# Optimization experiments

Hardware: AMD Instinct MI355X
Metric: run time of the kernel (lower is better)

## Reference

```python
import jax, jax.numpy as jnp
import numpy as np

B, N, D, H = 4, 256, 32, 512

def setup_inputs() -> dict:
    key = jax.random.key(0)
    ks = jax.random.split(key, 6)
    z = jax.random.normal(ks[0], (B, N, D), dtype=jnp.float32)
    motif_mask = (jax.random.uniform(ks[1], (B, N)) > 0.5).astype(jnp.float32)
    residue_mask = jnp.ones((B, N), dtype=jnp.float32)
    # Linear weights stored as (in, out); scaled like torch default init
    W1 = jax.random.normal(ks[2], (D * D, H), dtype=jnp.float32) / np.sqrt(D * D)
    b1 = jnp.zeros((H,), dtype=jnp.float32)
    W2 = jax.random.normal(ks[3], (H, H // 2), dtype=jnp.float32) / np.sqrt(H)
    b2 = jnp.zeros((H // 2,), dtype=jnp.float32)
    W3 = jax.random.normal(ks[4], (H // 2, 1), dtype=jnp.float32) / np.sqrt(H // 2)
    b3 = jnp.zeros((1,), dtype=jnp.float32)
    return {"z": z, "motif_mask": motif_mask, "residue_mask": residue_mask,
            "W1": W1, "b1": b1, "W2": W2, "b2": b2, "W3": W3, "b3": b3}

def reference(z, motif_mask, residue_mask, W1, b1, W2, b2, W3, b3):
    # kron[b,i,j, a*D+c] = z[b,i,a] * z[b,j,c]; first Linear on kron is the
    # bilinear form z_i^T W1_h z_j -- compute via two matmuls, never
    # materializing the (B,N,N,D^2) tensor.
    d = z.shape[-1]
    W1r = W1.reshape(d, d, -1)                      # (D, D, H); axis0 = z_i dim, axis1 = z_j dim
    tmp = jnp.einsum('bia,ach->bihc', z, W1r)        # (B, N, H, D)
    h1 = jax.nn.relu(jnp.einsum('bihc,bjc->bijh', tmp, z) + b1)  # (B, N, N, H)
    h2 = jax.nn.relu(jnp.einsum('bijh,hk->bijk', h1, W2) + b2)   # (B, N, N, H/2)
    contact_logits = (jnp.einsum('bijk,ko->bijo', h2, W3) + b3)[..., 0]  # (B, N, N)
    outer_mask = motif_mask[:, None, :] * motif_mask[:, :, None]
    contact_logits = contact_logits * outer_mask
    contact_map = jax.nn.sigmoid(contact_logits)
    return (contact_map, contact_logits)
```

## Files before the change

kernel.cpp:

```cpp
#include <hip/hip_runtime.h>
#include <hip/hip_bf16.h>
#include <cstdint>
#include <cstddef>

#define NB 4
#define NN 256
#define DD 32
#define HH 512

typedef __attribute__((ext_vector_type(8))) short short8;
typedef __attribute__((ext_vector_type(4))) float f32x4;
typedef __attribute__((ext_vector_type(16))) float f32x16;

static __device__ __forceinline__ unsigned cvtpk(float a, float b) {
  unsigned r;
  asm("v_cvt_pk_bf16_f32 %0, %1, %2" : "=v"(r) : "v"(a), "v"(b));
  return r;
}
static __device__ __forceinline__ unsigned short f2bf1(float a) {
  return (unsigned short)(cvtpk(a, 0.f) & 0xffffu);
}

static __device__ __forceinline__ short8 pack8(float4 a0, float4 a1) {
  union { unsigned u[4]; short8 s; } r;
  r.u[0] = cvtpk(a0.x, a0.y); r.u[1] = cvtpk(a0.z, a0.w);
  r.u[2] = cvtpk(a1.x, a1.y); r.u[3] = cvtpk(a1.z, a1.w);
  return r.s;
}

__global__ __launch_bounds__(256) void prep(const float* __restrict__ z,
                                            const float* __restrict__ W1,
                                            const float* __restrict__ W2,
                                            const float* __restrict__ motif,
                                            unsigned short* __restrict__ W2F,
                                            unsigned short* __restrict__ Tall,
                                            int* __restrict__ jlist,
                                            int* __restrict__ jcnt,
                                            int* __restrict__ wq,
                                            int* __restrict__ wqn) {
  const int blk = blockIdx.x;
  const int tid = threadIdx.x;
  if (blk < 512) {
    __shared__ unsigned short w1s[16384];
    const int nblk = blk >> 4, mgrp = blk & 15;
    const int bibase = mgrp * 64;

    #pragma unroll
    for (int r = 0; r < 16; ++r) {
      int task = r * 256 + tid;
      int row = task >> 2;
      int hq = task & 3;
      float4 v = *(const float4*)(W1 + (size_t)row * 512 + nblk * 16 + hq * 4);
      int a = row >> 5, c = row & 31;
      int quad = a >> 3, e = a & 7;
      float hv[4] = {v.x, v.y, v.z, v.w};
      #pragma unroll
      for (int vv = 0; vv < 4; ++vv) {
        int hl = hq * 4 + vv;
        int nl = hl * 32 + c;
        int w2 = nl >> 7, r7 = nl & 127;
        int l16 = r7 >> 3, nt = r7 & 7;
        w1s[((w2 * 8 + nt) * 64 + quad * 16 + l16) * 8 + e] = f2bf1(hv[vv]);
      }
    }
    __syncthreads();

    const int w2 = tid >> 6, lane = tid & 63;
    const int quad = lane >> 4, l16 = lane & 15;

    short8 bfr[8];
    #pragma unroll
    for (int nt = 0; nt < 8; ++nt)
      bfr[nt] = *(const short8*)&w1s[((w2 * 8 + nt) * 64 + lane) * 8];

    const int ncol = nblk * 512 + w2 * 128 + l16 * 8;
    #pragma unroll
    for (int mtg = 0; mtg < 2; ++mtg) {
      short8 afr[2];
      #pragma unroll
      for (int mi = 0; mi < 2; ++mi) {
        const float* zr = z + (size_t)(bibase + (mtg * 2 + mi) * 16 + l16) * 32 + quad * 8;
        float4 a0 = *(const float4*)(zr);
        float4 a1 = *(const float4*)(zr + 4);
        afr[mi] = pack8(a0, a1);
      }
      f32x4 d[2][8];
      #pragma unroll
      for (int mi = 0; mi < 2; ++mi)
        #pragma unroll
        for (int nt = 0; nt < 8; ++nt)
          d[mi][nt] = __builtin_amdgcn_mfma_f32_16x16x32_bf16(
              afr[mi], bfr[nt], (f32x4){0.f, 0.f, 0.f, 0.f}, 0, 0, 0);
      #pragma unroll
      for (int mi = 0; mi < 2; ++mi)
        #pragma unroll
        for (int r = 0; r < 4; ++r) {
          int rowbi = bibase + (mtg * 2 + mi) * 16 + quad * 4 + r;
          if (motif[rowbi] != 0.f) {
            uint4 p;
            p.x = cvtpk(d[mi][0][r], d[mi][1][r]);
            p.y = cvtpk(d[mi][2][r], d[mi][3][r]);
            p.z = cvtpk(d[mi][4][r], d[mi][5][r]);
            p.w = cvtpk(d[mi][6][r], d[mi][7][r]);
            *(uint4*)&Tall[(size_t)rowbi * 16384 + ncol] = p;
          }
        }
    }
  } else if (blk < 576) {
    int f8 = (blk - 512) * 256 + tid;
    int lane = f8 & 63;
    int nt = (f8 >> 6) & 1, s = (f8 >> 7) & 3, hc = (f8 >> 9) & 7, w = (f8 >> 12) & 3;
    int k2 = w * 64 + nt * 32 + (lane & 31);
    int hb = hc * 64 + s * 16 + (lane >> 5) * 8;
    float v[8];
    #pragma unroll
    for (int e = 0; e < 8; ++e) v[e] = W2[(hb + e) * 256 + k2];
    uint4 p;
    p.x = cvtpk(v[0], v[1]); p.y = cvtpk(v[2], v[3]);
    p.z = cvtpk(v[4], v[5]); p.w = cvtpk(v[6], v[7]);
    ((uint4*)W2F)[f8] = p;
  } else {
    __shared__ int itemc[4];
    __shared__ int baseh[4];
    const int w = tid >> 6, lane = tid & 63;
    int cnt = 0;
    if (w < NB) {
      #pragma unroll
      for (int ch = 0; ch < 4; ++ch) {
        int j = ch * 64 + lane;
        float m = motif[w * 256 + j];
        bool alive = (m != 0.f);
        unsigned long long mk = __ballot(alive);
        unsigned long long below = mk & ((1ull << lane) - 1ull);
        int pos = __popcll(below);
        if (alive) jlist[w * 256 + cnt + pos] = j;
        cnt += __popcll(mk);
      }
      if (lane == 0) {
        jcnt[w] = cnt;
        itemc[w] = cnt * ((cnt + 63) >> 6);
      }
    }
    __syncthreads();
    if (tid == 0) {
      int s = 0;
      #pragma unroll
      for (int k = 0; k < NB; ++k) { baseh[k] = s; s += itemc[k]; }
      *wqn = s;
    }
    __syncthreads();
    if (w < NB) {
      const int K = (cnt + 63) >> 6;
      const int base = baseh[w];
      int rank = 0;
      #pragma unroll
      for (int ch = 0; ch < 4; ++ch) {
        int i = ch * 64 + lane;
        bool alive = (motif[w * 256 + i] != 0.f);
        unsigned long long mk = __ballot(alive);
        unsigned long long below = mk & ((1ull << lane) - 1ull);
        int pos = __popcll(below);
        if (alive)
          for (int jt = 0; jt < K; ++jt)
            wq[base + (rank + pos) * K + jt] = (w * 256 + i) * 4 + jt;
        rank += __popcll(mk);
      }
    }
  }
}

__global__ __launch_bounds__(256) void fused(const unsigned short* __restrict__ Tall,
                                             const unsigned short* __restrict__ W2F,
                                             const float* __restrict__ z,
                                             const float* __restrict__ b1,
                                             const float* __restrict__ b2,
                                             const float* __restrict__ W3,
                                             const float* __restrict__ b3,
                                             const float* __restrict__ motif,
                                             const int* __restrict__ jlist,
                                             const int* __restrict__ jcnt,
                                             const int* __restrict__ wq,
                                             const int* __restrict__ wqn,
                                             float* __restrict__ out) {
  __shared__ unsigned short h1s[64 * 264];
  __shared__ float red[256];

  const int bx = blockIdx.x;
  const int tid = threadIdx.x;
  const size_t OUT2 = (size_t)NB * NN * NN;
  const int nq = *wqn;

  if (bx >= nq) {
    const int nf = (int)gridDim.x - nq;
    for (int p = (bx - nq) * 256 + tid; p < NB * NN * NN; p += nf * 256) {
      int bi = p >> 8, j = p & 255, b = bi >> 8;
      if (motif[bi] == 0.f || motif[b * 256 + j] == 0.f) {
        out[p] = 0.5f;
        out[OUT2 + p] = 0.f;
      }
    }
    return;
  }
  const int item = wq[bx];

  const int w = tid >> 6, lane = tid & 63;
  const int quad = lane >> 4, l16 = lane & 15;
  const int L = lane >> 5, c32 = lane & 31;

  const int bi = item >> 2, jt = item & 3;
  const int b = bi >> 8;
  const int cnt = jcnt[b];
  const int slotbase = jt * 64;
  const float mi_v = motif[bi];

  const unsigned short* Tbase = Tall + (size_t)bi * 16384 + (w * 16 + l16) * 32 + quad * 8;
  short8 tfr[8];
  #pragma unroll
  for (int q = 0; q < 8; ++q)
    tfr[q] = *(const short8*)(Tbase + q * 2048);

  short8 zfr[4];
  #pragma unroll
  for (int nt = 0; nt < 4; ++nt) {
    int slot = slotbase + nt * 16 + l16;
    int sc = slot < cnt ? slot : cnt - 1;
    int jj = jlist[b * 256 + sc] & 255;
    const float* zr = z + (size_t)(b * 256 + jj) * 32 + quad * 8;
    float4 a0 = *(const float4*)(zr);
    float4 a1 = *(const float4*)(zr + 4);
    zfr[nt] = pack8(a0, a1);
  }

  float b2v[2], w3v[2];
  #pragma unroll
  for (int nt = 0; nt < 2; ++nt) {
    int k2 = w * 64 + nt * 32 + c32;
    b2v[nt] = b2[k2];
    w3v[nt] = W3[k2];
  }

  f32x16 acc[2][2];
  #pragma unroll
  for (int mt = 0; mt < 2; ++mt)
    #pragma unroll
    for (int nt = 0; nt < 2; ++nt)
      acc[mt][nt] = (f32x16){0.f,0.f,0.f,0.f,0.f,0.f,0.f,0.f,
                             0.f,0.f,0.f,0.f,0.f,0.f,0.f,0.f};

  const unsigned short* Wp = W2F + w * 32768 + lane * 8;
  const float* b1base = b1 + w * 16 + quad * 4;

  #pragma unroll
  for (int half = 0; half < 2; ++half) {
    #pragma unroll
    for (int q = 0; q < 4; ++q) {
      float4 b1f = *(const float4*)(b1base + (half * 4 + q) * 64);
      f32x4 cin = {b1f.x, b1f.y, b1f.z, b1f.w};
      #pragma unroll
      for (int nt = 0; nt < 4; ++nt) {
        f32x4 d = __builtin_amdgcn_mfma_f32_16x16x32_bf16(
            tfr[half * 4 + q], zfr[nt], cin, 0, 0, 0);
        uint2 p;
        p.x = cvtpk(fmaxf(d[0], 0.f), fmaxf(d[1], 0.f));
        p.y = cvtpk(fmaxf(d[2], 0.f), fmaxf(d[3], 0.f));
        *(uint2*)&h1s[(nt * 16 + l16) * 264 + q * 64 + w * 16 + quad * 4] = p;
      }
    }
    __syncthreads();

    const unsigned short* Wh = Wp + half * 16384;
    const unsigned short* h1r = &h1s[c32 * 264 + L * 8];
    short8 bfp[3][2], afp[2][2];
    #pragma unroll
    for (int p = 0; p < 3; ++p) {
      bfp[p][0] = *(const short8*)(Wh + p * 1024);
      bfp[p][1] = *(const short8*)(Wh + p * 1024 + 512);
    }
    afp[0][0] = *(const short8*)(h1r);
    afp[0][1] = *(const short8*)(h1r + 32 * 264);
    afp[1][0] = *(const short8*)(h1r + 16);
    afp[1][1] = *(const short8*)(h1r + 32 * 264 + 16);
    #pragma unroll
    for (int u = 0; u < 16; ++u) {
      const int cur = u & 1, bq = u % 3;
      short8 a0 = afp[cur][0], a1 = afp[cur][1];
      short8 b0 = bfp[bq][0], b1q = bfp[bq][1];
      if (u < 14) {
        afp[cur][0] = *(const short8*)(h1r + (u + 2) * 16);
        afp[cur][1] = *(const short8*)(h1r + 32 * 264 + (u + 2) * 16);
      }
      if (u < 13) {
        bfp[bq][0] = *(const short8*)(Wh + (u + 3) * 1024);
        bfp[bq][1] = *(const short8*)(Wh + (u + 3) * 1024 + 512);
      }
      acc[0][0] = __builtin_amdgcn_mfma_f32_32x32x16_bf16(a0, b0, acc[0][0], 0, 0, 0);
      acc[0][1] = __builtin_amdgcn_mfma_f32_32x32x16_bf16(a0, b1q, acc[0][1], 0, 0, 0);
      acc[1][0] = __builtin_amdgcn_mfma_f32_32x32x16_bf16(a1, b0, acc[1][0], 0, 0, 0);
      acc[1][1] = __builtin_amdgcn_mfma_f32_32x32x16_bf16(a1, b1q, acc[1][1], 0, 0, 0);
    }
    if (half == 0) __syncthreads();
  }

  float pr[2][16];
  #pragma unroll
  for (int mt = 0; mt < 2; ++mt)
    #pragma unroll
    for (int reg = 0; reg < 16; ++reg) {
      float s = 0.f;
      #pragma unroll
      for (int nt = 0; nt < 2; ++nt) {
        float v = acc[mt][nt][reg] + b2v[nt];
        v = v > 0.f ? v : 0.f;
        s += v * w3v[nt];
      }
      s += __shfl_xor(s, 1);
      s += __shfl_xor(s, 2);
      s += __shfl_xor(s, 4);
      s += __shfl_xor(s, 8);
      s += __shfl_xor(s, 16);
      pr[mt][reg] = s;
    }
  if (c32 == 0) {
    #pragma unroll
    for (int mt = 0; mt < 2; ++mt)
      #pragma unroll
      for (int g = 0; g < 4; ++g) {
        float4 vv = {pr[mt][g * 4 + 0], pr[mt][g * 4 + 1],
                     pr[mt][g * 4 + 2], pr[mt][g * 4 + 3]};
        *(float4*)&red[w * 64 + mt * 32 + g * 8 + L * 4] = vv;
      }
  }
  __syncthreads();
  if (tid < 64) {
    int slot = slotbase + tid;
    if (slot < cnt) {
      int j = jlist[b * 256 + slot] & 255;
      float logit = red[tid] + red[64 + tid] + red[128 + tid] + red[192 + tid] + b3[0];
      float mm = mi_v * motif[b * 256 + j];
      logit *= mm;
      float map = 1.f / (1.f + expf(-logit));
      size_t idx = (size_t)bi * 256 + j;
      out[idx] = map;
      out[OUT2 + idx] = logit;
    }
  }
}

extern "C" void kernel_launch(void* const* d_in, const int* in_sizes, int n_in,
                              void* d_out, int out_size, void* d_ws, size_t ws_size,
                              hipStream_t stream) {
  const float* z     = (const float*)d_in[0];
  const float* motif = (const float*)d_in[1];
  const float* W1 = (const float*)d_in[3];
  const float* b1 = (const float*)d_in[4];
  const float* W2 = (const float*)d_in[5];
  const float* b2 = (const float*)d_in[6];
  const float* W3 = (const float*)d_in[7];
  const float* b3 = (const float*)d_in[8];
  float* out = (float*)d_out;

  char* ws = (char*)d_ws;
  unsigned short* Tall = (unsigned short*)ws;
  unsigned short* W2F  = (unsigned short*)(ws + 33554432);
  int* jlist = (int*)(ws + 33554432 + 262144);
  int* jcnt  = (int*)(ws + 33554432 + 262144 + 4096);
  int* wq    = (int*)(ws + 33554432 + 262144 + 4096 + 64);
  int* wqn   = (int*)(ws + 33554432 + 262144 + 4096 + 64 + 16384);

  prep<<<577, 256, 0, stream>>>(z, W1, W2, motif, W2F, Tall,
                                jlist, jcnt, wq, wqn);
  fused<<<4096, 256, 0, stream>>>(Tall, W2F, z, b1, b2, W3, b3, motif,
                                  jlist, jcnt, wq, wqn, out);
}
```

Measured before the change: 127.2 us.

## Split W1 bf16 repack into own kernel, move mask fill to prep, deepen prefetch

W1 is now converted to a bf16 fragment layout once by a new prep0 kernel, replacing the per-block shared-memory transpose that 512 blocks each repeated. The fill of masked output entries moves from idle fused blocks into extra prep1 blocks. The work-queue order for two-tile rows is permuted in groups of 16, and the W2 fragment prefetch in the second GEMM goes from three to four stages. This adds a kernel launch and a 1 MB workspace buffer, and uses more registers for the deeper prefetch.

New measurement: 119.0 us. -6.4%, faster.

```diff
diff --git a/kernel.cpp b/kernel.cpp
--- a/kernel.cpp
+++ b/kernel.cpp
@@ -28,50 +28,52 @@
   return r.s;
 }
 
-__global__ __launch_bounds__(256) void prep(const float* __restrict__ z,
-                                            const float* __restrict__ W1,
-                                            const float* __restrict__ W2,
-                                            const float* __restrict__ motif,
-                                            unsigned short* __restrict__ W2F,
-                                            unsigned short* __restrict__ Tall,
-                                            int* __restrict__ jlist,
-                                            int* __restrict__ jcnt,
-                                            int* __restrict__ wq,
-                                            int* __restrict__ wqn) {
+__global__ __launch_bounds__(256) void prep0(const float* __restrict__ W1,
+                                             unsigned short* __restrict__ W1F) {
+  const int f = blockIdx.x * 256 + threadIdx.x;
+  #pragma unroll
+  for (int r = 0; r < 4; ++r) {
+    int row = r * 16384 + f;
+    int lane = row & 63;
+    int nt = (row >> 6) & 7, w2 = (row >> 9) & 3, nblk = row >> 11;
+    int quad = lane >> 4, l16 = lane & 15;
+    int nl = w2 * 128 + l16 * 8 + nt;
+    int hl = nl >> 5, c = nl & 31;
+    const float* src = W1 + (size_t)(nblk * 16 + hl);
+    float v[8];
+    #pragma unroll
+    for (int e = 0; e < 8; ++e)
+      v[e] = src[(size_t)((quad * 8 + e) * 32 + c) * 512];
+    uint4 p;
+    p.x = cvtpk(v[0], v[1]); p.y = cvtpk(v[2], v[3]);
+    p.z = cvtpk(v[4], v[5]); p.w = cvtpk(v[6], v[7]);
+    *(uint4*)&W1F[(size_t)row * 8] = p;
+  }
+}
+
+__global__ __launch_bounds__(256) void prep1(const float* __restrict__ z,
+                                             const unsigned short* __restrict__ W1F,
+                                             const float* __restrict__ W2,
+                                             const float* __restrict__ motif,
+                                             unsigned short* __restrict__ W2F,
+                                             unsigned short* __restrict__ Tall,
+                                             int* __restrict__ jlist,
+                                             int* __restrict__ jcnt,
+                                             int* __restrict__ wq,
+                                             int* __restrict__ wqn,
+                                             float* __restrict__ out) {
   const int blk = blockIdx.x;
   const int tid = threadIdx.x;
   if (blk < 512) {
-    __shared__ unsigned short w1s[16384];
     const int nblk = blk >> 4, mgrp = blk & 15;
     const int bibase = mgrp * 64;
-
-    #pragma unroll
-    for (int r = 0; r < 16; ++r) {
-      int task = r * 256 + tid;
-      int row = task >> 2;
-      int hq = task & 3;
-      float4 v = *(const float4*)(W1 + (size_t)row * 512 + nblk * 16 + hq * 4);
-      int a = row >> 5, c = row & 31;
-      int quad = a >> 3, e = a & 7;
-      float hv[4] = {v.x, v.y, v.z, v.w};
-      #pragma unroll
-      for (int vv = 0; vv < 4; ++vv) {
-        int hl = hq * 4 + vv;
-        int nl = hl * 32 + c;
-        int w2 = nl >> 7, r7 = nl & 127;
-        int l16 = r7 >> 3, nt = r7 & 7;
-        w1s[((w2 * 8 + nt) * 64 + quad * 16 + l16) * 8 + e] = f2bf1(hv[vv]);
-      }
-    }
-    __syncthreads();
-
     const int w2 = tid >> 6, lane = tid & 63;
     const int quad = lane >> 4, l16 = lane & 15;
 
     short8 bfr[8];
     #pragma unroll
     for (int nt = 0; nt < 8; ++nt)
-      bfr[nt] = *(const short8*)&w1s[((w2 * 8 + nt) * 64 + lane) * 8];
+      bfr[nt] = *(const short8*)&W1F[(size_t)((((nblk * 4 + w2) * 8) + nt) * 64 + lane) * 8];
 
     const int ncol = nblk * 512 + w2 * 128 + l16 * 8;
     #pragma unroll
@@ -119,7 +121,7 @@
     p.x = cvtpk(v[0], v[1]); p.y = cvtpk(v[2], v[3]);
     p.z = cvtpk(v[4], v[5]); p.w = cvtpk(v[6], v[7]);
     ((uint4*)W2F)[f8] = p;
-  } else {
+  } else if (blk == 576) {
     __shared__ int itemc[4];
     __shared__ int baseh[4];
     const int w = tid >> 6, lane = tid & 63;
@@ -152,6 +154,7 @@
     if (w < NB) {
       const int K = (cnt + 63) >> 6;
       const int base = baseh[w];
+      const int L2n = cnt * K;
       int rank = 0;
       #pragma unroll
       for (int ch = 0; ch < 4; ++ch) {
@@ -160,10 +163,30 @@
         unsigned long long mk = __ballot(alive);
         unsigned long long below = mk & ((1ull << lane) - 1ull);
         int pos = __popcll(below);
-        if (alive)
-          for (int jt = 0; jt < K; ++jt)
-            wq[base + (rank + pos) * K + jt] = (w * 256 + i) * 4 + jt;
+        if (alive) {
+          int idx0 = (rank + pos) * K;
+          for (int jt = 0; jt < K; ++jt) {
+            int idx = idx0 + jt;
+            int nidx = idx;
+            if (K == 2) {
+              int g = idx >> 4;
+              if (g * 16 + 16 <= L2n)
+                nidx = g * 16 + ((idx & 1) << 3) + ((idx >> 1) & 7);
+            }
+            wq[base + nidx] = (w * 256 + i) * 4 + jt;
+          }
+        }
         rank += __popcll(mk);
+      }
+    }
+  } else {
+    const size_t OUT2 = (size_t)NB * NN * NN;
+    const int c = blk - 577;
+    for (int p = c * 4096 + tid; p < (c + 1) * 4096; p += 256) {
+      int bi = p >> 8, j = p & 255, b = bi >> 8;
+      if (motif[bi] == 0.f || motif[b * 256 + j] == 0.f) {
+        out[p] = 0.5f;
+        out[OUT2 + p] = 0.f;
       }
     }
   }
@@ -190,17 +213,7 @@
   const size_t OUT2 = (size_t)NB * NN * NN;
   const int nq = *wqn;
 
-  if (bx >= nq) {
-    const int nf = (int)gridDim.x - nq;
-    for (int p = (bx - nq) * 256 + tid; p < NB * NN * NN; p += nf * 256) {
-      int bi = p >> 8, j = p & 255, b = bi >> 8;
-      if (motif[bi] == 0.f || motif[b * 256 + j] == 0.f) {
-        out[p] = 0.5f;
-        out[OUT2 + p] = 0.f;
-      }
-    }
-    return;
-  }
+  if (bx >= nq) return;
   const int item = wq[bx];
 
   const int w = tid >> 6, lane = tid & 63;
@@ -270,9 +283,9 @@
 
     const unsigned short* Wh = Wp + half * 16384;
     const unsigned short* h1r = &h1s[c32 * 264 + L * 8];
-    short8 bfp[3][2], afp[2][2];
-    #pragma unroll
-    for (int p = 0; p < 3; ++p) {
+    short8 bfp[4][2], afp[2][2];
+    #pragma unroll
+    for (int p = 0; p < 4; ++p) {
       bfp[p][0] = *(const short8*)(Wh + p * 1024);
       bfp[p][1] = *(const short8*)(Wh + p * 1024 + 512);
     }
@@ -282,16 +295,16 @@
     afp[1][1] = *(const short8*)(h1r + 32 * 264 + 16);
     #pragma unroll
     for (int u = 0; u < 16; ++u) {
-      const int cur = u & 1, bq = u % 3;
+      const int cur = u & 1, bq = u & 3;
       short8 a0 = afp[cur][0], a1 = afp[cur][1];
       short8 b0 = bfp[bq][0], b1q = bfp[bq][1];
       if (u < 14) {
         afp[cur][0] = *(const short8*)(h1r + (u + 2) * 16);
         afp[cur][1] = *(const short8*)(h1r + 32 * 264 + (u + 2) * 16);
       }
-      if (u < 13) {
-        bfp[bq][0] = *(const short8*)(Wh + (u + 3) * 1024);
-        bfp[bq][1] = *(const short8*)(Wh + (u + 3) * 1024 + 512);
+      if (u < 12) {
+        bfp[bq][0] = *(const short8*)(Wh + (u + 4) * 1024);
+        bfp[bq][1] = *(const short8*)(Wh + (u + 4) * 1024 + 512);
       }
       acc[0][0] = __builtin_amdgcn_mfma_f32_32x32x16_bf16(a0, b0, acc[0][0], 0, 0, 0);
       acc[0][1] = __builtin_amdgcn_mfma_f32_32x32x16_bf16(a0, b1q, acc[0][1], 0, 0, 0);
@@ -362,13 +375,16 @@
   char* ws = (char*)d_ws;
   unsigned short* Tall = (unsigned short*)ws;
   unsigned short* W2F  = (unsigned short*)(ws + 33554432);
-  int* jlist = (int*)(ws + 33554432 + 262144);
-  int* jcnt  = (int*)(ws + 33554432 + 262144 + 4096);
-  int* wq    = (int*)(ws + 33554432 + 262144 + 4096 + 64);
-  int* wqn   = (int*)(ws + 33554432 + 262144 + 4096 + 64 + 16384);
-
-  prep<<<577, 256, 0, stream>>>(z, W1, W2, motif, W2F, Tall,
-                                jlist, jcnt, wq, wqn);
+  unsigned short* W1F  = (unsigned short*)(ws + 33554432 + 262144);
+  char* tail = ws + 33554432 + 262144 + 1048576;
+  int* jlist = (int*)(tail);
+  int* jcnt  = (int*)(tail + 4096);
+  int* wq    = (int*)(tail + 4096 + 64);
+  int* wqn   = (int*)(tail + 4096 + 64 + 16384);
+
+  prep0<<<64, 256, 0, stream>>>(W1, W1F);
+  prep1<<<641, 256, 0, stream>>>(z, W1F, W2, motif, W2F, Tall,
+                                 jlist, jcnt, wq, wqn, out);
   fused<<<4096, 256, 0, stream>>>(Tall, W2F, z, b1, b2, W3, b3, motif,
                                   jlist, jcnt, wq, wqn, out);
 }
```
